# Optimization experiments

Measured on AMD Instinct MI355X. Metric: run time of the kernel, lower is better.

The kernel has to match this reference:

```python
import jax, jax.numpy as jnp
import numpy as np

DMODEL = 1024
NHEAD = 16
HDIM = DMODEL // NHEAD
CTXLEN = 2048
BATCH = 2


def setup_inputs() -> dict:
    key = jax.random.key(0)
    k_x, k_qkv, k_pw, k_pb = jax.random.split(key, 4)
    x = jax.random.normal(k_x, (BATCH, CTXLEN, DMODEL), dtype=jnp.float32)
    # nn.Linear weights: stored as [out, in]; init scale ~ 1/sqrt(in)
    s = 1.0 / np.sqrt(DMODEL)
    w_qkv = jax.random.uniform(k_qkv, (3 * DMODEL, DMODEL), minval=-s, maxval=s, dtype=jnp.float32)
    w_proj = jax.random.uniform(k_pw, (DMODEL, DMODEL), minval=-s, maxval=s, dtype=jnp.float32)
    b_proj = jax.random.uniform(k_pb, (DMODEL,), minval=-s, maxval=s, dtype=jnp.float32)
    return {"x": x, "w_qkv": w_qkv, "w_proj": w_proj, "b_proj": b_proj}


def reference(x, w_qkv, w_proj, b_proj):
    b, t, c = x.shape
    qkv = jnp.einsum('btc,oc->bto', x, w_qkv)  # [b, t, 3c]
    q, k, v = jnp.split(qkv, 3, axis=-1)
    # [b, nhead, t, hdim]
    q = q.reshape(b, t, NHEAD, HDIM).transpose(0, 2, 1, 3)
    k = k.reshape(b, t, NHEAD, HDIM).transpose(0, 2, 1, 3)
    v = v.reshape(b, t, NHEAD, HDIM).transpose(0, 2, 1, 3)
    # NOTE: original code MULTIPLIES by sqrt(hdim) (not the usual divide)
    att = jnp.einsum('bhqd,bhkd->bhqk', q, k) * (HDIM ** 0.5)
    causal = jnp.tril(jnp.ones((t, t), dtype=bool))  # [t, t]
    att = jnp.where(causal[None, None], att, -jnp.inf)
    att = jax.nn.softmax(att, axis=-1)
    y = jnp.einsum('bhqk,bhkd->bhqd', att, v)
    y = y.transpose(0, 2, 1, 3).reshape(b, t, c)
    return jnp.einsum('btc,oc->bto', y, w_proj) + b_proj
```

## Files before the change

### kernel.cpp

```cpp
#include <hip/hip_runtime.h>
#include <hip/hip_bf16.h>

#define DMODEL 1024
#define NHEAD 16
#define HDIM 64
#define CTXLEN 2048
#define BATCH 2
#define M_TOTAL (BATCH * CTXLEN)

typedef unsigned short ushort_t;
typedef __attribute__((ext_vector_type(8))) _Float16 f16x8;
typedef __attribute__((ext_vector_type(8))) unsigned short u16x8;
typedef __attribute__((ext_vector_type(4))) float f32x4;
typedef __attribute__((ext_vector_type(4))) unsigned short u16x4;

__device__ __forceinline__ unsigned short f32_f16(float f) {
    return __builtin_bit_cast(unsigned short, (_Float16)f);
}
__device__ __forceinline__ float f16_f32(unsigned short h) {
    return (float)__builtin_bit_cast(_Float16, h);
}
__device__ __forceinline__ float fast_exp2(float x) {
    return __builtin_amdgcn_exp2f(x);
}
__device__ __forceinline__ f32x4 mfma16f(f16x8 a, f16x8 b, f32x4 c) {
    return __builtin_amdgcn_mfma_f32_16x16x32_f16(a, b, c, 0, 0, 0);
}
__device__ __forceinline__ void gload_lds16(const ushort_t* g, ushort_t* l) {
    __builtin_amdgcn_global_load_lds(
        (const __attribute__((address_space(1))) void*)g,
        (__attribute__((address_space(3))) void*)l, 16, 0, 0);
}
__device__ __forceinline__ int unit_off(int qt) {
    if (qt < 8)  return qt;
    if (qt < 16) return 8 + (qt - 8) * 2;
    if (qt < 24) return 24 + (qt - 16) * 3;
    return 48 + (qt - 24) * 4;
}

__global__ __launch_bounds__(256)
void conv3_f32_f16(const float* __restrict__ a, ushort_t* __restrict__ da, int na4,
                   const float* __restrict__ b, ushort_t* __restrict__ db, int nb4,
                   const float* __restrict__ c, ushort_t* __restrict__ dc, int nc4) {
    const int n = na4 + nb4 + nc4;
    for (int i = blockIdx.x * blockDim.x + threadIdx.x; i < n;
         i += gridDim.x * blockDim.x) {
        const float* s; ushort_t* d; int j = i;
        if (j < na4) { s = a; d = da; }
        else if (j - na4 < nb4) { j -= na4; s = b; d = db; }
        else { j -= na4 + nb4; s = c; d = dc; }
        const float4 v = reinterpret_cast<const float4*>(s)[j];
        u16x4 o;
        o[0] = f32_f16(v.x); o[1] = f32_f16(v.y);
        o[2] = f32_f16(v.z); o[3] = f32_f16(v.w);
        reinterpret_cast<u16x4*>(d)[j] = o;
    }
}

template<int BN, bool QKV_EPI>
__global__ __launch_bounds__(256)
void gemm_f16_nt(const ushort_t* __restrict__ A, const ushort_t* __restrict__ B,
                 const float* __restrict__ bias, float* __restrict__ C,
                 ushort_t* __restrict__ qf, ushort_t* __restrict__ kf,
                 ushort_t* __restrict__ vb,
                 int M, int N, int K) {
    constexpr int NF = BN / 32;
    constexpr int BOFF = 4096;
    __shared__ ushort_t lds[BOFF + BN * 32];

    const int tid  = threadIdx.x;
    const int lane = tid & 63;
    const int wave = tid >> 6;
    const int lc   = lane & 15;
    const int lg   = lane >> 4;
    const int wr   = wave >> 1;
    const int wc   = wave & 1;
    const int row0 = blockIdx.y * 128;
    const int col0 = blockIdx.x * BN;

    const int c0 = tid, c1 = 256 + tid;
    const int r0 = c0 >> 2, l0 = (c0 & 3) ^ ((c0 >> 3) & 3);
    const int r1 = c1 >> 2, l1 = (c1 & 3) ^ ((c1 >> 3) & 3);
    const size_t gaoff0 = (size_t)(row0 + r0) * K + l0 * 8;
    const size_t gaoff1 = (size_t)(row0 + r1) * K + l1 * 8;
    const size_t gboff0 = (size_t)(col0 + r0) * K + l0 * 8;
    const size_t gboff1 = (size_t)(col0 + r1) * K + l1 * 8;
    const int ld0 = c0 * 8, ld1 = c1 * 8;

    int aoff[4], boff[NF];
    #pragma unroll
    for (int m = 0; m < 4; ++m) {
        const int ra = wr * 64 + m * 16 + lc;
        aoff[m] = ra * 32 + ((lg ^ ((ra >> 1) & 3)) * 8);
    }
    #pragma unroll
    for (int n = 0; n < NF; ++n) {
        const int rb = wc * (NF * 16) + n * 16 + lc;
        boff[n] = rb * 32 + ((lg ^ ((rb >> 1) & 3)) * 8);
    }

    f32x4 acc[4][NF];
    const f32x4 zero4 = {0.f, 0.f, 0.f, 0.f};
    #pragma unroll
    for (int m = 0; m < 4; ++m)
        #pragma unroll
        for (int n = 0; n < NF; ++n) acc[m][n] = zero4;

    const int NT = K >> 5;

    auto stage = [&](int kt) {
        const int ko = kt * 32;
        gload_lds16(A + gaoff0 + ko, &lds[ld0]);
        gload_lds16(A + gaoff1 + ko, &lds[ld1]);
        gload_lds16(B + gboff0 + ko, &lds[BOFF + ld0]);
        if (BN == 128) gload_lds16(B + gboff1 + ko, &lds[BOFF + ld1]);
    };

    stage(0);
    for (int kt = 0; kt < NT; ++kt) {
        __syncthreads();
        f16x8 fa[4], fb[NF];
        #pragma unroll
        for (int m = 0; m < 4; ++m)
            fa[m] = *reinterpret_cast<const f16x8*>(&lds[aoff[m]]);
        #pragma unroll
        for (int n = 0; n < NF; ++n)
            fb[n] = *reinterpret_cast<const f16x8*>(&lds[BOFF + boff[n]]);
        __syncthreads();
        if (kt + 1 < NT) stage(kt + 1);
        #pragma unroll
        for (int m = 0; m < 4; ++m)
            #pragma unroll
            for (int n = 0; n < NF; ++n)
                acc[m][n] = mfma16f(fa[m], fb[n], acc[m][n]);
    }

    if (!QKV_EPI) {
        #pragma unroll
        for (int m = 0; m < 4; ++m)
            #pragma unroll
            for (int i = 0; i < 4; ++i) {
                const int r = row0 + wr * 64 + m * 16 + lg * 4 + i;
                #pragma unroll
                for (int n = 0; n < NF; ++n) {
                    const int c = col0 + wc * (NF * 16) + n * 16 + lc;
                    C[(size_t)r * N + c] = acc[m][n][i] + bias[c];
                }
            }
    } else {
        #pragma unroll
        for (int m = 0; m < 4; ++m)
            #pragma unroll
            for (int i = 0; i < 4; ++i) {
                const int r = row0 + wr * 64 + m * 16 + lg * 4 + i;
                const int bb = r >> 11;
                const int t  = r & 2047;
                #pragma unroll
                for (int n = 0; n < NF; ++n) {
                    const int cg  = col0 + wc * (NF * 16) + n * 16 + lc;
                    const int sec = cg >> 10;
                    const int ch  = cg & 1023;
                    const int hh  = ch >> 6;
                    const int d   = ch & 63;
                    const size_t off = (((size_t)(bb * NHEAD + hh)) * CTXLEN + t) * HDIM + d;
                    const unsigned short hv = f32_f16(acc[m][n][i]);
                    if (sec == 0)      qf[off] = hv;
                    else if (sec == 1) kf[off] = hv;
                    else               vb[off] = hv;
                }
            }
    }
}

__global__ __launch_bounds__(256)
void transpose_v(const ushort_t* __restrict__ vb, ushort_t* __restrict__ vt) {
    __shared__ ushort_t T[64][66];
    const int tt = blockIdx.x;
    const int bh = blockIdx.y;
    const int tid = threadIdx.x;
    const int r  = tid >> 2;
    const int c0 = (tid & 3) * 16;

    const ushort_t* src = vb + ((size_t)bh * CTXLEN + tt * 64) * HDIM;
    #pragma unroll
    for (int half = 0; half < 2; ++half) {
        const u16x8 v = *reinterpret_cast<const u16x8*>(&src[(size_t)r * HDIM + c0 + half * 8]);
        #pragma unroll
        for (int j = 0; j < 8; ++j) T[r][c0 + half * 8 + j] = v[j];
    }
    __syncthreads();
    ushort_t* dst = vt + ((size_t)bh * HDIM + r) * CTXLEN + tt * 64 + c0;
    u16x8 o0, o1;
    #pragma unroll
    for (int j = 0; j < 8; ++j) { o0[j] = T[c0 + j][r]; o1[j] = T[c0 + 8 + j][r]; }
    *reinterpret_cast<u16x8*>(&dst[0]) = o0;
    *reinterpret_cast<u16x8*>(&dst[8]) = o1;
}

#define SCALE_LOG2 11.5415603271f

__global__ __launch_bounds__(256)
void attn_fwd7(const ushort_t* __restrict__ qf, const ushort_t* __restrict__ kf,
               const ushort_t* __restrict__ vt,
               ushort_t* __restrict__ py, float* __restrict__ pml) {
    __shared__ ushort_t KH[2][4096];
    __shared__ ushort_t VT[2][4096];
    __shared__ ushort_t Ps[4][16][64];

    const int id    = blockIdx.x;
    const int bh    = id & 31;
    const int u_off = 79 - (id >> 5);
    int qt, u;
    if (u_off < 8)       { qt = u_off;                          u = 0; }
    else if (u_off < 24) { const int t = u_off - 8;  qt = 8  + (t >> 1); u = t & 1; }
    else if (u_off < 48) { const int t = u_off - 24; const int q3 = t / 3; qt = 16 + q3; u = t - q3 * 3; }
    else                 { const int t = u_off - 48; qt = 24 + (t >> 2); u = t & 3; }
    const int total = qt + 1;
    const int nu    = (qt >> 3) + 1;
    const int base  = total / nu, rem = total % nu;
    const int kb0   = u * base + (u < rem ? u : rem);
    const int len   = base + (u < rem ? 1 : 0);
    const int slot  = bh * 80 + u_off;

    const int tid  = threadIdx.x;
    const int wave = tid >> 6;
    const int lane = tid & 63;
    const int lc   = lane & 15;
    const int lg   = lane >> 4;

    const ushort_t* kfb = kf + (size_t)bh * CTXLEN * HDIM;
    const ushort_t* vtb = vt + (size_t)bh * HDIM * CTXLEN;

    const int cA = tid, cB = 256 + tid;
    const int rA = cA >> 3, sgA = (cA & 7) ^ (rA & 7);
    const int rB = cB >> 3, sgB = (cB & 7) ^ (rB & 7);

    auto stage = [&](int kb, int buf) {
        const size_t koff = (size_t)(kb * 64);
        gload_lds16(kfb + (koff + rA) * HDIM + sgA * 8, &KH[buf][cA * 8]);
        gload_lds16(kfb + (koff + rB) * HDIM + sgB * 8, &KH[buf][cB * 8]);
        gload_lds16(vtb + (size_t)rA * CTXLEN + kb * 64 + sgA * 8, &VT[buf][cA * 8]);
        gload_lds16(vtb + (size_t)rB * CTXLEN + kb * 64 + sgB * 8, &VT[buf][cB * 8]);
    };

    const size_t qrow = (size_t)bh * CTXLEN + qt * 64 + wave * 16 + lc;
    f16x8 qfr[2];
    #pragma unroll
    for (int ds = 0; ds < 2; ++ds)
        qfr[ds] = *reinterpret_cast<const f16x8*>(&qf[qrow * HDIM + ds * 32 + lg * 8]);

    const f32x4 zero4 = {0.f, 0.f, 0.f, 0.f};
    f32x4 yacc[4];
    #pragma unroll
    for (int t = 0; t < 4; ++t) yacc[t] = zero4;
    float m_i = -1e30f, l_i = 0.f;

    stage(kb0, 0);
    __syncthreads();

    int cur = 0;
    for (int s = 0; s < len; ++s) {
        const int kb = kb0 + s;
        if (s + 1 < len) stage(kb + 1, cur ^ 1);

        f16x8 kfr[4][2];
        #pragma unroll
        for (int tc = 0; tc < 4; ++tc) {
            const int rk = tc * 16 + lc;
            #pragma unroll
            for (int ds = 0; ds < 2; ++ds) {
                const int a = rk * 64 + (((ds * 4 + lg) ^ (rk & 7)) * 8);
                kfr[tc][ds] = *reinterpret_cast<const f16x8*>(&KH[cur][a]);
            }
        }
        f16x8 vf[4][2];
        #pragma unroll
        for (int t = 0; t < 4; ++t) {
            const int rv = t * 16 + lc;
            #pragma unroll
            for (int ks = 0; ks < 2; ++ks) {
                const int a = rv * 64 + (((ks * 4 + lg) ^ (rv & 7)) * 8);
                vf[t][ks] = *reinterpret_cast<const f16x8*>(&VT[cur][a]);
            }
        }

        f32x4 sacc[4];
        #pragma unroll
        for (int tc = 0; tc < 4; ++tc) sacc[tc] = zero4;
        __builtin_amdgcn_s_setprio(1);
        #pragma unroll
        for (int tc = 0; tc < 4; ++tc)
            #pragma unroll
            for (int ds = 0; ds < 2; ++ds)
                sacc[tc] = mfma16f(kfr[tc][ds], qfr[ds], sacc[tc]);
        __builtin_amdgcn_s_setprio(0);

        float p[4][4];
        #pragma unroll
        for (int tc = 0; tc < 4; ++tc)
            #pragma unroll
            for (int i = 0; i < 4; ++i)
                p[tc][i] = sacc[tc][i] * SCALE_LOG2;
        if (kb == qt) {
            const int q_loc = wave * 16 + lc;
            #pragma unroll
            for (int tc = 0; tc < 4; ++tc)
                #pragma unroll
                for (int i = 0; i < 4; ++i)
                    if ((tc * 16 + lg * 4 + i) > q_loc) p[tc][i] = -1e30f;
        }
        float mx = p[0][0];
        #pragma unroll
        for (int tc = 0; tc < 4; ++tc)
            #pragma unroll
            for (int i = 0; i < 4; ++i) mx = fmaxf(mx, p[tc][i]);
        mx = fmaxf(mx, __shfl_xor(mx, 16));
        mx = fmaxf(mx, __shfl_xor(mx, 32));

        if (__all(mx <= m_i + 8.0f)) {
            float psum = 0.f;
            #pragma unroll
            for (int tc = 0; tc < 4; ++tc)
                #pragma unroll
                for (int i = 0; i < 4; ++i) {
                    const float e = fast_exp2(p[tc][i] - m_i);
                    p[tc][i] = e;
                    psum += e;
                }
            psum += __shfl_xor(psum, 16);
            psum += __shfl_xor(psum, 32);
            l_i += psum;
        } else {
            const float mnew = fmaxf(m_i, mx);
            const float corr = fast_exp2(m_i - mnew);
            float psum = 0.f;
            #pragma unroll
            for (int tc = 0; tc < 4; ++tc)
                #pragma unroll
                for (int i = 0; i < 4; ++i) {
                    const float e = fast_exp2(p[tc][i] - mnew);
                    p[tc][i] = e;
                    psum += e;
                }
            psum += __shfl_xor(psum, 16);
            psum += __shfl_xor(psum, 32);
            l_i = l_i * corr + psum;
            m_i = mnew;
            #pragma unroll
            for (int t = 0; t < 4; ++t) yacc[t] *= corr;
        }

        #pragma unroll
        for (int tc = 0; tc < 4; ++tc) {
            const int eb = tc * 16 + lg * 4;
            const int se = ((((eb >> 3) ^ (lc & 7)) << 3) | (eb & 7));
            u16x4 pk;
            #pragma unroll
            for (int i = 0; i < 4; ++i) pk[i] = f32_f16(p[tc][i]);
            *reinterpret_cast<u16x4*>(&Ps[wave][lc][se]) = pk;
        }
        f16x8 pa[2];
        #pragma unroll
        for (int ks = 0; ks < 2; ++ks) {
            const int sl = ((ks * 4 + lg) ^ (lc & 7)) << 3;
            pa[ks] = *reinterpret_cast<const f16x8*>(&Ps[wave][lc][sl]);
        }
        __builtin_amdgcn_s_setprio(1);
        #pragma unroll
        for (int t = 0; t < 4; ++t)
            #pragma unroll
            for (int ks = 0; ks < 2; ++ks)
                yacc[t] = mfma16f(vf[t][ks], pa[ks], yacc[t]);
        __builtin_amdgcn_s_setprio(0);

        __syncthreads();
        cur ^= 1;
    }

    const int row = wave * 16 + lc;
    ushort_t* prow = py + ((size_t)slot * 64 + row) * 64;
    #pragma unroll
    for (int t = 0; t < 4; ++t) {
        u16x4 o;
        #pragma unroll
        for (int i = 0; i < 4; ++i) o[i] = f32_f16(yacc[t][i]);
        *reinterpret_cast<u16x4*>(&prow[t * 16 + lg * 4]) = o;
    }
    if (lg == 0) {
        pml[(size_t)slot * 128 + row]      = m_i;
        pml[(size_t)slot * 128 + 64 + row] = l_i;
    }
}

__global__ __launch_bounds__(256)
void merge_attn(const ushort_t* __restrict__ py, const float* __restrict__ pml,
                ushort_t* __restrict__ yb) {
    const int bid = blockIdx.x;
    const int bh  = bid >> 5;
    const int qt  = bid & 31;
    const int b   = bh >> 4;
    const int h   = bh & 15;
    const int tid = threadIdx.x;
    const int row = tid >> 2;
    const int d0  = (tid & 3) * 16;

    const int nu    = (qt >> 3) + 1;
    const int sbase = bh * 80 + unit_off(qt);

    float mu[4], lu[4];
    float M = -1e30f;
    #pragma unroll
    for (int u = 0; u < 4; ++u) {
        if (u < nu) {
            mu[u] = pml[(size_t)(sbase + u) * 128 + row];
            lu[u] = pml[(size_t)(sbase + u) * 128 + 64 + row];
            M = fmaxf(M, mu[u]);
        } else { mu[u] = -1e30f; lu[u] = 0.f; }
    }
    float w[4], ltot = 0.f;
    #pragma unroll
    for (int u = 0; u < 4; ++u) {
        w[u] = (u < nu) ? fast_exp2(mu[u] - M) : 0.f;
        ltot += w[u] * lu[u];
    }

    float y[16];
    #pragma unroll
    for (int j = 0; j < 16; ++j) y[j] = 0.f;
    #pragma unroll
    for (int u = 0; u < 4; ++u) {
        if (u < nu) {
            const ushort_t* pr = py + ((size_t)(sbase + u) * 64 + row) * 64 + d0;
            const u16x8 a = *reinterpret_cast<const u16x8*>(&pr[0]);
            const u16x8 c = *reinterpret_cast<const u16x8*>(&pr[8]);
            #pragma unroll
            for (int j = 0; j < 8; ++j) {
                y[j]     += w[u] * f16_f32(a[j]);
                y[8 + j] += w[u] * f16_f32(c[j]);
            }
        }
    }
    const float inv = 1.0f / ltot;
    ushort_t* dst = yb + (size_t)(b * CTXLEN + qt * 64 + row) * DMODEL + h * HDIM + d0;
    u16x8 o0, o1;
    #pragma unroll
    for (int j = 0; j < 8; ++j) {
        o0[j] = f32_f16(y[j] * inv);
        o1[j] = f32_f16(y[8 + j] * inv);
    }
    *reinterpret_cast<u16x8*>(&dst[0]) = o0;
    *reinterpret_cast<u16x8*>(&dst[8]) = o1;
}

extern "C" void kernel_launch(void* const* d_in, const int* in_sizes, int n_in,
                              void* d_out, int out_size, void* d_ws, size_t ws_size,
                              hipStream_t stream) {
    const float* x      = (const float*)d_in[0];
    const float* w_qkv  = (const float*)d_in[1];
    const float* w_proj = (const float*)d_in[2];
    const float* b_proj = (const float*)d_in[3];
    float* out = (float*)d_out;

    char* ws = (char*)d_ws;
    ushort_t* wqf = (ushort_t*)(ws);
    ushort_t* wpf = (ushort_t*)(ws + 6291456);
    ushort_t* xf  = (ushort_t*)(ws + 8388608);
    ushort_t* qf  = (ushort_t*)(ws + 16777216);
    ushort_t* kf  = (ushort_t*)(ws + 25165824);
    ushort_t* vb  = (ushort_t*)(ws + 33554432);
    ushort_t* vt  = (ushort_t*)(ws + 41943040);
    ushort_t* py  = (ushort_t*)(ws + 50331648);
    float*    pml = (float*)   (ws + 71303168);
    ushort_t* yb  = xf;

    const dim3 blk(256);

    conv3_f32_f16<<<dim3(2048), blk, 0, stream>>>(
        x, xf, M_TOTAL * DMODEL / 4,
        w_qkv, wqf, 3 * DMODEL * DMODEL / 4,
        w_proj, wpf, DMODEL * DMODEL / 4);

    gemm_f16_nt<128, true><<<dim3(3 * DMODEL / 128, M_TOTAL / 128), blk, 0, stream>>>(
        xf, wqf, nullptr, nullptr, qf, kf, vb, M_TOTAL, 3 * DMODEL, DMODEL);

    transpose_v<<<dim3(CTXLEN / 64, BATCH * NHEAD), blk, 0, stream>>>(vb, vt);

    attn_fwd7<<<dim3(2560), blk, 0, stream>>>(qf, kf, vt, py, pml);
    merge_attn<<<dim3(1024), blk, 0, stream>>>(py, pml, yb);

    gemm_f16_nt<64, false><<<dim3(DMODEL / 64, M_TOTAL / 128), blk, 0, stream>>>(
        yb, wpf, b_proj, out, nullptr, nullptr, nullptr, M_TOTAL, DMODEL, DMODEL);
}
```

Measured before the change: 120.6 us.

## Switch attention kernel to 32x32 MFMA with two waves and register-resident P

```diff
diff --git a/kernel.cpp b/kernel.cpp
--- a/kernel.cpp
+++ b/kernel.cpp
@@ -10,9 +10,13 @@
 
 typedef unsigned short ushort_t;
 typedef __attribute__((ext_vector_type(8))) _Float16 f16x8;
+typedef __attribute__((ext_vector_type(2))) _Float16 f16x2;
 typedef __attribute__((ext_vector_type(8))) unsigned short u16x8;
 typedef __attribute__((ext_vector_type(4))) float f32x4;
+typedef __attribute__((ext_vector_type(16))) float f32x16;
 typedef __attribute__((ext_vector_type(4))) unsigned short u16x4;
+typedef __attribute__((ext_vector_type(4))) unsigned int u32x4;
+typedef __attribute__((ext_vector_type(2))) unsigned int u32x2;
 
 __device__ __forceinline__ unsigned short f32_f16(float f) {
     return __builtin_bit_cast(unsigned short, (_Float16)f);
@@ -25,6 +29,9 @@
 }
 __device__ __forceinline__ f32x4 mfma16f(f16x8 a, f16x8 b, f32x4 c) {
     return __builtin_amdgcn_mfma_f32_16x16x32_f16(a, b, c, 0, 0, 0);
+}
+__device__ __forceinline__ f32x16 mfma32f(f16x8 a, f16x8 b, f32x16 c) {
+    return __builtin_amdgcn_mfma_f32_32x32x16_f16(a, b, c, 0, 0, 0);
 }
 __device__ __forceinline__ void gload_lds16(const ushort_t* g, ushort_t* l) {
     __builtin_amdgcn_global_load_lds(
@@ -199,13 +206,12 @@
 
 #define SCALE_LOG2 11.5415603271f
 
-__global__ __launch_bounds__(256)
-void attn_fwd7(const ushort_t* __restrict__ qf, const ushort_t* __restrict__ kf,
-               const ushort_t* __restrict__ vt,
-               ushort_t* __restrict__ py, float* __restrict__ pml) {
+__global__ __launch_bounds__(128)
+void attn_fwd10(const ushort_t* __restrict__ qf, const ushort_t* __restrict__ kf,
+                const ushort_t* __restrict__ vt,
+                ushort_t* __restrict__ py, float* __restrict__ pml) {
     __shared__ ushort_t KH[2][4096];
     __shared__ ushort_t VT[2][4096];
-    __shared__ ushort_t Ps[4][16][64];
 
     const int id    = blockIdx.x;
     const int bh    = id & 31;
@@ -225,34 +231,35 @@
     const int tid  = threadIdx.x;
     const int wave = tid >> 6;
     const int lane = tid & 63;
-    const int lc   = lane & 15;
-    const int lg   = lane >> 4;
+    const int lq   = lane & 31;
+    const int h    = lane >> 5;
 
     const ushort_t* kfb = kf + (size_t)bh * CTXLEN * HDIM;
     const ushort_t* vtb = vt + (size_t)bh * HDIM * CTXLEN;
 
-    const int cA = tid, cB = 256 + tid;
-    const int rA = cA >> 3, sgA = (cA & 7) ^ (rA & 7);
-    const int rB = cB >> 3, sgB = (cB & 7) ^ (rB & 7);
-
     auto stage = [&](int kb, int buf) {
         const size_t koff = (size_t)(kb * 64);
-        gload_lds16(kfb + (koff + rA) * HDIM + sgA * 8, &KH[buf][cA * 8]);
-        gload_lds16(kfb + (koff + rB) * HDIM + sgB * 8, &KH[buf][cB * 8]);
-        gload_lds16(vtb + (size_t)rA * CTXLEN + kb * 64 + sgA * 8, &VT[buf][cA * 8]);
-        gload_lds16(vtb + (size_t)rB * CTXLEN + kb * 64 + sgB * 8, &VT[buf][cB * 8]);
+        #pragma unroll
+        for (int i = 0; i < 4; ++i) {
+            const int c  = tid + i * 128;
+            const int r  = c >> 3;
+            const int sg = (c & 7) ^ (r & 7);
+            gload_lds16(kfb + (koff + r) * HDIM + sg * 8, &KH[buf][c * 8]);
+            gload_lds16(vtb + (size_t)r * CTXLEN + kb * 64 + sg * 8, &VT[buf][c * 8]);
+        }
     };
 
-    const size_t qrow = (size_t)bh * CTXLEN + qt * 64 + wave * 16 + lc;
-    f16x8 qfr[2];
-    #pragma unroll
-    for (int ds = 0; ds < 2; ++ds)
-        qfr[ds] = *reinterpret_cast<const f16x8*>(&qf[qrow * HDIM + ds * 32 + lg * 8]);
-
-    const f32x4 zero4 = {0.f, 0.f, 0.f, 0.f};
-    f32x4 yacc[4];
-    #pragma unroll
-    for (int t = 0; t < 4; ++t) yacc[t] = zero4;
+    const size_t qrow = (size_t)bh * CTXLEN + qt * 64 + wave * 32 + lq;
+    f16x8 qfr[4];
+    #pragma unroll
+    for (int ds = 0; ds < 4; ++ds)
+        qfr[ds] = *reinterpret_cast<const f16x8*>(&qf[qrow * HDIM + ds * 16 + h * 8]);
+
+    f32x16 yacc[2];
+    #pragma unroll
+    for (int db = 0; db < 2; ++db)
+        #pragma unroll
+        for (int r = 0; r < 16; ++r) yacc[db][r] = 0.f;
     float m_i = -1e30f, l_i = 0.f;
 
     stage(kb0, 0);
@@ -263,71 +270,73 @@
         const int kb = kb0 + s;
         if (s + 1 < len) stage(kb + 1, cur ^ 1);
 
-        f16x8 kfr[4][2];
-        #pragma unroll
-        for (int tc = 0; tc < 4; ++tc) {
-            const int rk = tc * 16 + lc;
-            #pragma unroll
-            for (int ds = 0; ds < 2; ++ds) {
-                const int a = rk * 64 + (((ds * 4 + lg) ^ (rk & 7)) * 8);
-                kfr[tc][ds] = *reinterpret_cast<const f16x8*>(&KH[cur][a]);
+        f16x8 kfr[2][4];
+        #pragma unroll
+        for (int kb2 = 0; kb2 < 2; ++kb2) {
+            const int row = kb2 * 32 + lq;
+            #pragma unroll
+            for (int ds = 0; ds < 4; ++ds) {
+                const int ch = (ds * 2 + h) ^ (row & 7);
+                kfr[kb2][ds] = *reinterpret_cast<const f16x8*>(&KH[cur][row * 64 + ch * 8]);
             }
         }
-        f16x8 vf[4][2];
-        #pragma unroll
-        for (int t = 0; t < 4; ++t) {
-            const int rv = t * 16 + lc;
-            #pragma unroll
-            for (int ks = 0; ks < 2; ++ks) {
-                const int a = rv * 64 + (((ks * 4 + lg) ^ (rv & 7)) * 8);
-                vf[t][ks] = *reinterpret_cast<const f16x8*>(&VT[cur][a]);
+        f16x8 vfr[2][4];
+        #pragma unroll
+        for (int db = 0; db < 2; ++db) {
+            const int row = db * 32 + lq;
+            #pragma unroll
+            for (int ks = 0; ks < 4; ++ks) {
+                const int ch = (ks * 2 + h) ^ (row & 7);
+                vfr[db][ks] = *reinterpret_cast<const f16x8*>(&VT[cur][row * 64 + ch * 8]);
             }
         }
 
-        f32x4 sacc[4];
-        #pragma unroll
-        for (int tc = 0; tc < 4; ++tc) sacc[tc] = zero4;
+        f32x16 sacc[2];
+        #pragma unroll
+        for (int kb2 = 0; kb2 < 2; ++kb2)
+            #pragma unroll
+            for (int r = 0; r < 16; ++r) sacc[kb2][r] = 0.f;
         __builtin_amdgcn_s_setprio(1);
         #pragma unroll
-        for (int tc = 0; tc < 4; ++tc)
-            #pragma unroll
-            for (int ds = 0; ds < 2; ++ds)
-                sacc[tc] = mfma16f(kfr[tc][ds], qfr[ds], sacc[tc]);
+        for (int kb2 = 0; kb2 < 2; ++kb2)
+            #pragma unroll
+            for (int ds = 0; ds < 4; ++ds)
+                sacc[kb2] = mfma32f(kfr[kb2][ds], qfr[ds], sacc[kb2]);
         __builtin_amdgcn_s_setprio(0);
 
-        float p[4][4];
-        #pragma unroll
-        for (int tc = 0; tc < 4; ++tc)
-            #pragma unroll
-            for (int i = 0; i < 4; ++i)
-                p[tc][i] = sacc[tc][i] * SCALE_LOG2;
+        float p[2][16];
+        #pragma unroll
+        for (int kb2 = 0; kb2 < 2; ++kb2)
+            #pragma unroll
+            for (int r = 0; r < 16; ++r)
+                p[kb2][r] = sacc[kb2][r] * SCALE_LOG2;
         if (kb == qt) {
-            const int q_loc = wave * 16 + lc;
-            #pragma unroll
-            for (int tc = 0; tc < 4; ++tc)
+            const int q_loc = wave * 32 + lq;
+            #pragma unroll
+            for (int kb2 = 0; kb2 < 2; ++kb2)
                 #pragma unroll
-                for (int i = 0; i < 4; ++i)
-                    if ((tc * 16 + lg * 4 + i) > q_loc) p[tc][i] = -1e30f;
+                for (int r = 0; r < 16; ++r) {
+                    const int k_rel = kb2 * 32 + (r & 3) + 8 * (r >> 2) + 4 * h;
+                    if (k_rel > q_loc) p[kb2][r] = -1e30f;
+                }
         }
         float mx = p[0][0];
         #pragma unroll
-        for (int tc = 0; tc < 4; ++tc)
-            #pragma unroll
-            for (int i = 0; i < 4; ++i) mx = fmaxf(mx, p[tc][i]);
-        mx = fmaxf(mx, __shfl_xor(mx, 16));
+        for (int kb2 = 0; kb2 < 2; ++kb2)
+            #pragma unroll
+            for (int r = 0; r < 16; ++r) mx = fmaxf(mx, p[kb2][r]);
         mx = fmaxf(mx, __shfl_xor(mx, 32));
 
         if (__all(mx <= m_i + 8.0f)) {
             float psum = 0.f;
             #pragma unroll
-            for (int tc = 0; tc < 4; ++tc)
+            for (int kb2 = 0; kb2 < 2; ++kb2)
                 #pragma unroll
-                for (int i = 0; i < 4; ++i) {
-                    const float e = fast_exp2(p[tc][i] - m_i);
-                    p[tc][i] = e;
+                for (int r = 0; r < 16; ++r) {
+                    const float e = fast_exp2(p[kb2][r] - m_i);
+                    p[kb2][r] = e;
                     psum += e;
                 }
-            psum += __shfl_xor(psum, 16);
             psum += __shfl_xor(psum, 32);
             l_i += psum;
         } else {
@@ -335,60 +344,68 @@
             const float corr = fast_exp2(m_i - mnew);
             float psum = 0.f;
             #pragma unroll
-            for (int tc = 0; tc < 4; ++tc)
+            for (int kb2 = 0; kb2 < 2; ++kb2)
                 #pragma unroll
-                for (int i = 0; i < 4; ++i) {
-                    const float e = fast_exp2(p[tc][i] - mnew);
-                    p[tc][i] = e;
+                for (int r = 0; r < 16; ++r) {
+                    const float e = fast_exp2(p[kb2][r] - mnew);
+                    p[kb2][r] = e;
                     psum += e;
                 }
-            psum += __shfl_xor(psum, 16);
             psum += __shfl_xor(psum, 32);
             l_i = l_i * corr + psum;
             m_i = mnew;
             #pragma unroll
-            for (int t = 0; t < 4; ++t) yacc[t] *= corr;
-        }
-
-        #pragma unroll
-        for (int tc = 0; tc < 4; ++tc) {
-            const int eb = tc * 16 + lg * 4;
-            const int se = ((((eb >> 3) ^ (lc & 7)) << 3) | (eb & 7));
-            u16x4 pk;
-            #pragma unroll
-            for (int i = 0; i < 4; ++i) pk[i] = f32_f16(p[tc][i]);
-            *reinterpret_cast<u16x4*>(&Ps[wave][lc][se]) = pk;
-        }
-        f16x8 pa[2];
-        #pragma unroll
-        for (int ks = 0; ks < 2; ++ks) {
-            const int sl = ((ks * 4 + lg) ^ (lc & 7)) << 3;
-            pa[ks] = *reinterpret_cast<const f16x8*>(&Ps[wave][lc][sl]);
-        }
+            for (int db = 0; db < 2; ++db)
+                #pragma unroll
+                for (int r = 0; r < 16; ++r) yacc[db][r] *= corr;
+        }
+
+        f16x8 pfr[4];
+        #pragma unroll
+        for (int kb2 = 0; kb2 < 2; ++kb2) {
+            unsigned pk[8];
+            #pragma unroll
+            for (int j = 0; j < 8; ++j)
+                pk[j] = __builtin_bit_cast(unsigned,
+                    __builtin_amdgcn_cvt_pkrtz(p[kb2][2 * j], p[kb2][2 * j + 1]));
+            #pragma unroll
+            for (int half = 0; half < 2; ++half) {
+                const u32x2 sw0 = __builtin_amdgcn_permlane32_swap(
+                    pk[half * 4 + 0], pk[half * 4 + 2], false, false);
+                const u32x2 sw1 = __builtin_amdgcn_permlane32_swap(
+                    pk[half * 4 + 1], pk[half * 4 + 3], false, false);
+                u32x4 f;
+                f[0] = sw0[0]; f[1] = sw1[0]; f[2] = sw0[1]; f[3] = sw1[1];
+                pfr[kb2 * 2 + half] = __builtin_bit_cast(f16x8, f);
+            }
+        }
+
         __builtin_amdgcn_s_setprio(1);
         #pragma unroll
-        for (int t = 0; t < 4; ++t)
-            #pragma unroll
-            for (int ks = 0; ks < 2; ++ks)
-                yacc[t] = mfma16f(vf[t][ks], pa[ks], yacc[t]);
+        for (int db = 0; db < 2; ++db)
+            #pragma unroll
+            for (int ks = 0; ks < 4; ++ks)
+                yacc[db] = mfma32f(vfr[db][ks], pfr[ks], yacc[db]);
         __builtin_amdgcn_s_setprio(0);
 
         __syncthreads();
         cur ^= 1;
     }
 
-    const int row = wave * 16 + lc;
-    ushort_t* prow = py + ((size_t)slot * 64 + row) * 64;
-    #pragma unroll
-    for (int t = 0; t < 4; ++t) {
-        u16x4 o;
-        #pragma unroll
-        for (int i = 0; i < 4; ++i) o[i] = f32_f16(yacc[t][i]);
-        *reinterpret_cast<u16x4*>(&prow[t * 16 + lg * 4]) = o;
-    }
-    if (lg == 0) {
-        pml[(size_t)slot * 128 + row]      = m_i;
-        pml[(size_t)slot * 128 + 64 + row] = l_i;
+    const int q_loc = wave * 32 + lq;
+    ushort_t* prow = py + ((size_t)slot * 64 + q_loc) * 64;
+    #pragma unroll
+    for (int db = 0; db < 2; ++db)
+        #pragma unroll
+        for (int r4 = 0; r4 < 4; ++r4) {
+            u16x4 o;
+            #pragma unroll
+            for (int e = 0; e < 4; ++e) o[e] = f32_f16(yacc[db][r4 * 4 + e]);
+            *reinterpret_cast<u16x4*>(&prow[db * 32 + r4 * 8 + h * 4]) = o;
+        }
+    if (h == 0) {
+        pml[(size_t)slot * 128 + q_loc]      = m_i;
+        pml[(size_t)slot * 128 + 64 + q_loc] = l_i;
     }
 }
 
@@ -485,7 +502,7 @@
 
     transpose_v<<<dim3(CTXLEN / 64, BATCH * NHEAD), blk, 0, stream>>>(vb, vt);
 
-    attn_fwd7<<<dim3(2560), blk, 0, stream>>>(qf, kf, vt, py, pml);
+    attn_fwd10<<<dim3(2560), dim3(128), 0, stream>>>(qf, kf, vt, py, pml);
     merge_attn<<<dim3(1024), blk, 0, stream>>>(py, pml, yb);
 
     gemm_f16_nt<64, false><<<dim3(DMODEL / 64, M_TOTAL / 128), blk, 0, stream>>>(
```

Result: no change. 122.8 us (+1.8%).
